# Optimization experiments

Hardware: AMD Instinct MI355X
Metric: run time of the kernel (lower is better)

The kernel has to match this reference:

```python
import jax, jax.numpy as jnp
import numpy as np

N_NODES = 16000
N_EDGES = 256000
F = 128        # invariant edge feature dim
MUL = 64       # multiplicity of env/V irreps (mul_gcd)
HID = 128      # mlp_n_hidden
SQRT3 = float(np.sqrt(3.0))

# e3nn-style activation normalization constant for silu:
# c = sqrt(E_{z~N(0,1)}[silu(z)^2]), so silu(z)/c has unit second moment.
_z = np.linspace(-12.0, 12.0, 100001)
_pdf = np.exp(-0.5 * _z ** 2) / np.sqrt(2.0 * np.pi)
_silu = _z / (1.0 + np.exp(-_z))
SILU_C = float(np.sqrt(np.trapz(_silu ** 2 * _pdf, _z)))


def _nsilu(x):
    return jax.nn.silu(x) / SILU_C


def _lin(x, W):
    # e3nn 'path' gradient normalization: W ~ N(0,1), forward scaled by 1/sqrt(fan_in)
    return (x @ W) / jnp.sqrt(jnp.asarray(W.shape[0], x.dtype))


def setup_inputs() -> dict:
    key = jax.random.key(0)
    ks = jax.random.split(key, 11)
    inp = {
        'vectors': jax.random.normal(ks[0], (N_EDGES, 3), jnp.float32),
        'x': jax.random.normal(ks[1], (N_EDGES, F), jnp.float32),
        'V': jax.random.normal(ks[2], (N_EDGES, 4 * MUL), jnp.float32),  # 64x0e + 64x1o
        'u': jax.random.uniform(ks[3], (N_EDGES,), jnp.float32),
        'm': jnp.ones((N_EDGES,), jnp.float32),
        'W_env': jax.random.normal(ks[4], (F, 2 * MUL), jnp.float32),
        'W1': jax.random.normal(ks[5], (F + 2 * MUL, HID), jnp.float32),
        'W2': jax.random.normal(ks[6], (HID, HID), jnp.float32),
        'W3': jax.random.normal(ks[7], (HID, HID), jnp.float32),
        'W_out': jax.random.normal(ks[8], (2 * MUL, MUL), jnp.float32),
        'senders': jax.random.randint(ks[9], (N_EDGES,), 0, N_NODES, jnp.int32),
    }
    return inp


def reference(vectors, x, V, u, m, W_env, W1, W2, W3, W_out, senders):
    E = vectors.shape[0]
    x = x * m[:, None]

    # n_neighbors = scatter_sum(m, dst=senders, map_back=True)
    n_neighbors = jax.ops.segment_sum(m, senders, num_segments=N_NODES)[senders]  # (E,)

    # w = Linear(num_irreps=2*MUL)(x)
    w = _lin(x, W_env)                  # (E, 128)
    w0, w1 = w[:, :MUL], w[:, MUL:]     # scalar / vector channel weights

    # spherical harmonics (component normalization): Y0 = 1, Y1 = sqrt(3)*rhat
    rhat = vectors / jnp.linalg.norm(vectors, axis=-1, keepdims=True)
    Y1 = SQRT3 * rhat                   # (E, 3)

    # w * Y * m, scatter_sum over senders, map back, normalize by n_neighbors
    denom = n_neighbors + 1e-5
    ws = w0 * m[:, None]                                   # (E, MUL)   w * Y0
    wv = (w1[:, :, None] * Y1[:, None, :]) * m[:, None, None]  # (E, MUL, 3)
    wY_s = jax.ops.segment_sum(ws, senders, num_segments=N_NODES)[senders] / denom[:, None]
    wY_v = jax.ops.segment_sum(wv, senders, num_segments=N_NODES)[senders] / denom[:, None, None]

    # V.mul_to_axis(): (E, MUL, 0e+1o)
    Vs = V[:, :MUL]                      # (E, MUL)
    Vv = V[:, MUL:].reshape(E, MUL, 3)   # (E, MUL, 3)

    # tensor product, filter_ir_out = {0e, 1o} (CG, component normalization)
    s_a = wY_s * Vs                                  # 0e x 0e -> 0e
    s_b = jnp.sum(wY_v * Vv, axis=-1) / SQRT3        # 1o x 1o -> 0e
    v_a = wY_s[:, :, None] * Vv                      # 0e x 1o -> 1o
    v_b = wY_v * Vs[:, :, None]                      # 1o x 0e -> 1o

    # scalars -> concatenated into x; vectors stay equivariant
    x = jnp.concatenate([x, s_a, s_b], axis=1)       # (E, F + 2*MUL)

    # invariant MLP (silu, no output activation)
    h = _nsilu(_lin(x, W1))
    h = _nsilu(_lin(h, W2))
    h = _lin(h, W3)                                  # (E, HID)
    x_out = u[:, None] * h

    # Linear(irreps_out=64x1o) on 128x1o
    V_in = jnp.concatenate([v_a, v_b], axis=1)       # (E, 2*MUL, 3)
    V_out = jnp.einsum('euk,uo->eok', V_in, W_out) / jnp.sqrt(jnp.asarray(2 * MUL, V.dtype))
    V_out = V_out.reshape(E, MUL * 3)                # (E, 192)

    return x_out, V_out
```

## Files before the change

### kernel.cpp

```cpp
#include <hip/hip_runtime.h>
#include <math.h>

typedef short bf16x8 __attribute__((ext_vector_type(8)));
typedef float f32x4 __attribute__((ext_vector_type(4)));

#define S128 0.08838834764831845f
#define S256I 0.0625f
#define NN_NODES 16000

#define WS_COUNTS   16448000
#define WS_OFFSETS  (WS_COUNTS + 64000)
#define WS_CURSOR   (WS_OFFSETS + 64000)
#define WS_INV      (WS_CURSOR + 64000)
#define WS_W1 (WS_INV + 1024000)
#define WS_W2 (WS_W1 + 65536)
#define WS_W3 (WS_W2 + 32768)
#define WS_WO (WS_W3 + 32768)
#define WS_WE (WS_WO + 16384)
#define WS_VECM (WS_WE + 32768)
#define WS_XMB  (WS_VECM + 4096000)

static float compute_inv_silu_c() {
    double sum = 0.0, prev = 0.0;
    const double dz = 24.0 / 100000.0;
    for (int i = 0; i <= 100000; ++i) {
        double z = -12.0 + dz * (double)i;
        double pdf = exp(-0.5 * z * z) * 0.3989422804014327;
        double s = z / (1.0 + exp(-z));
        double f = s * s * pdf;
        if (i) sum += 0.5 * (prev + f) * dz;
        prev = f;
    }
    return (float)(1.0 / sqrt(sum));
}
static const float INV_SILU_C = compute_inv_silu_c();

__device__ __forceinline__ unsigned int packbf(float a, float b) {
    union { float f; unsigned int u; } ca, cb;
    ca.f = a; cb.f = b;
    unsigned int ua = ca.u + (0x7fffu + ((ca.u >> 16) & 1u));
    unsigned int ub = cb.u + (0x7fffu + ((cb.u >> 16) & 1u));
    return (ua >> 16) | (ub & 0xffff0000u);
}
__device__ __forceinline__ unsigned short bf16r(float v) {
    union { float f; unsigned int u; } c; c.f = v;
    return (unsigned short)((c.u + (0x7fffu + ((c.u >> 16) & 1u))) >> 16);
}
__device__ __forceinline__ float bflo(unsigned int u) { return __uint_as_float(u << 16); }
__device__ __forceinline__ float bfhi(unsigned int u) { return __uint_as_float(u & 0xffff0000u); }
__device__ __forceinline__ int swz(int row, int b) { return b ^ ((row & 15) << 4); }
__device__ __forceinline__ float nsilu(float v, float ic) {
    return v / (1.0f + __expf(-v)) * ic;
}

__global__ __launch_bounds__(256) void k_wprep(
    const float* __restrict__ W1, const float* __restrict__ W2,
    const float* __restrict__ W3, const float* __restrict__ Wout,
    const float* __restrict__ Wenv, char* __restrict__ wsb)
{
    const int t = blockIdx.x * 256 + threadIdx.x;
    if (t < NN_NODES) ((int*)(wsb + WS_COUNTS))[t] = 0;
    if (t < 32768) {
        int n = t & 127, k = t >> 7;
        *(unsigned short*)(wsb + WS_W1 + n * 512 + k * 2) =
            bf16r(W1[k * 128 + n] * S256I);
    }
    if (t < 16384) {
        int n = t & 127, k = t >> 7;
        *(unsigned short*)(wsb + WS_W2 + n * 256 + k * 2) =
            bf16r(W2[k * 128 + n] * S128);
        *(unsigned short*)(wsb + WS_W3 + n * 256 + k * 2) =
            bf16r(W3[k * 128 + n] * S128);
    }
    if (t < 16384) {
        int j = t & 127, k = t >> 7;
        int c = (j & 1) ? 64 + (j >> 1) : (j >> 1);
        *(unsigned short*)(wsb + WS_WE + j * 256 + k * 2) =
            bf16r(Wenv[k * 128 + c] * S128);
    }
    if (t < 8192) {
        int o = t & 63, uu = t >> 6;
        *(unsigned short*)(wsb + WS_WO + o * 256 + ((uu * 2) ^ ((o & 15) << 4))) =
            bf16r(Wout[uu * 64 + o] * S128);
    }
}

__global__ __launch_bounds__(1024) void k_hist(
    const int* __restrict__ senders, int* __restrict__ counts, int E)
{
    const int e = blockIdx.x * 1024 + threadIdx.x;
    if (e < E) atomicAdd(&counts[senders[e]], 1);
}

__global__ __launch_bounds__(1024) void k_scan(
    const int* __restrict__ counts, int* __restrict__ offsets,
    int* __restrict__ cursor)
{
    __shared__ int part[1024];
    const int t = threadIdx.x;
    const int s0 = t * 16;
    const int s1 = (s0 + 16 < NN_NODES) ? s0 + 16 : NN_NODES;
    int s = 0;
    for (int i = s0; i < s1; ++i) s += counts[i];
    part[t] = s;
    __syncthreads();
    for (int off = 1; off < 1024; off <<= 1) {
        int v = part[t];
        if (t >= off) v += part[t - off];
        __syncthreads();
        part[t] = v;
        __syncthreads();
    }
    int run = t ? part[t - 1] : 0;
    for (int i = s0; i < s1; ++i) {
        offsets[i] = run; cursor[i] = run; run += counts[i];
    }
}

__global__ __launch_bounds__(1024) void k_binfill(
    const int* __restrict__ senders, const float* __restrict__ vectors,
    const float* __restrict__ m, int* __restrict__ cursor,
    int* __restrict__ inv, float4* __restrict__ vecm, int E)
{
    const int e = blockIdx.x * 1024 + threadIdx.x;
    if (e < E) {
        const int p = atomicAdd(&cursor[senders[e]], 1);
        inv[e] = p;
        float4 vm;
        vm.x = vectors[(size_t)e * 3 + 0];
        vm.y = vectors[(size_t)e * 3 + 1];
        vm.z = vectors[(size_t)e * 3 + 2];
        vm.w = m[e];
        vecm[p] = vm;
    }
}

__global__ __launch_bounds__(512) void k_env(
    const float* __restrict__ x, const float* __restrict__ m,
    const char* __restrict__ wsb, const int* __restrict__ inv,
    char* __restrict__ wout, char* __restrict__ xmb, int E)
{
    __shared__ char lds[32768];
    const int tid = threadIdx.x, l = tid & 63, wid = tid >> 6;
    const int lr = l & 15, lg = l >> 4;
    const int n0 = wid * 16;

    bf16x8 B[4];
    #pragma unroll
    for (int kk = 0; kk < 4; ++kk)
        B[kk] = *(const bf16x8*)(wsb + WS_WE + (n0 + lr) * 256 + kk * 64 + lg * 16);

    const int eb = blockIdx.x * 128;
    {
        const int el = tid >> 2, q = tid & 3;
        const int e = eb + el;
        if (e < E) {
            const float mv = m[e];
            const float4* xp = (const float4*)&x[(size_t)e * 128 + q * 32];
            #pragma unroll
            for (int j = 0; j < 4; ++j) {
                float4 A = xp[2 * j], Bv = xp[2 * j + 1];
                int4 w;
                w.x = packbf(A.x * mv, A.y * mv); w.y = packbf(A.z * mv, A.w * mv);
                w.z = packbf(Bv.x * mv, Bv.y * mv); w.w = packbf(Bv.z * mv, Bv.w * mv);
                *(int4*)(lds + el * 256 + swz(el, q * 64 + j * 16)) = w;
            }
        } else {
            const int4 z = {0, 0, 0, 0};
            #pragma unroll
            for (int j = 0; j < 4; ++j)
                *(int4*)(lds + el * 256 + swz(el, q * 64 + j * 16)) = z;
        }
    }
    __syncthreads();

    {
        const int el = tid >> 2, q = tid & 3;
        const int e = eb + el;
        if (e < E) {
            int4* d = (int4*)(xmb + (size_t)e * 256 + q * 64);
            #pragma unroll
            for (int j = 0; j < 4; ++j)
                d[j] = *(int4*)(lds + el * 256 + swz(el, q * 64 + j * 16));
        }
    }

    f32x4 acc[8];
    #pragma unroll
    for (int a = 0; a < 8; ++a) acc[a] = (f32x4){0.f, 0.f, 0.f, 0.f};

    #pragma unroll
    for (int kk = 0; kk < 4; ++kk) {
        const int kb = kk * 64 + lg * 16;
        #pragma unroll
        for (int mt = 0; mt < 8; ++mt) {
            const int row = mt * 16 + lr;
            bf16x8 a = *(const bf16x8*)(lds + row * 256 + swz(row, kb));
            acc[mt] = __builtin_amdgcn_mfma_f32_16x16x32_bf16(a, B[kk], acc[mt], 0, 0, 0);
        }
    }
    __syncthreads();

    #pragma unroll
    for (int mt = 0; mt < 8; ++mt)
        #pragma unroll
        for (int r = 0; r < 4; ++r) {
            const int row = mt * 16 + lg * 4 + r;
            *(unsigned short*)(lds + row * 256 + swz(row, (n0 + lr) * 2)) =
                bf16r(acc[mt][r]);
        }
    __syncthreads();

    {
        const int el = tid >> 2, q = tid & 3;
        const int e = eb + el;
        if (e < E) {
            const int p = inv[e];
            int4* d = (int4*)(wout + (size_t)p * 256 + q * 64);
            #pragma unroll
            for (int j = 0; j < 4; ++j)
                d[j] = *(int4*)(lds + el * 256 + swz(el, q * 64 + j * 16));
        }
    }
}

__global__ __launch_bounds__(256) void k_gather(
    const char* __restrict__ wvb, const float4* __restrict__ vecm,
    const int* __restrict__ counts, const int* __restrict__ offsets,
    float* __restrict__ node_cnt, float* __restrict__ node_s,
    float* __restrict__ node_v)
{
    const int l = threadIdx.x & 63, wid = threadIdx.x >> 6;
    const int n = blockIdx.x * 4 + wid;
    if (n >= NN_NODES) return;
    const int cnt = counts[n], base = offsets[n];

    float as = 0.f, a0 = 0.f, a1 = 0.f, a2 = 0.f, am = 0.f;
    for (int i = 0; i < cnt; ++i) {
        const unsigned int wv =
            *(const unsigned int*)(wvb + (size_t)(base + i) * 256 + l * 4);
        const float4 vm = vecm[base + i];
        const float rn = 1.7320508075688772f /
                         sqrtf(vm.x * vm.x + vm.y * vm.y + vm.z * vm.z);
        const float w0 = bflo(wv) * vm.w;
        const float c1 = bfhi(wv) * vm.w * rn;
        as += w0; am += vm.w;
        a0 += c1 * vm.x; a1 += c1 * vm.y; a2 += c1 * vm.z;
    }
    if (l == 0) node_cnt[n] = am;
    node_s[(size_t)n * 64 + l] = as;
    float* nv = &node_v[((size_t)n * 64 + l) * 3];
    nv[0] = a0; nv[1] = a1; nv[2] = a2;
}

__global__ __launch_bounds__(512, 4) void k_fuse(
    const float* __restrict__ V, const int* __restrict__ senders,
    const float* __restrict__ node_cnt, const float* __restrict__ node_s,
    const float* __restrict__ node_v, const char* __restrict__ wsb,
    const char* __restrict__ xmb, const float* __restrict__ ug,
    float* __restrict__ out_x, float* __restrict__ out_v,
    float inv_c, int E)
{
    __shared__ char lds[81920];
    const int tid = threadIdx.x, l = tid & 63, wid = tid >> 6;
    const int lr = l & 15, lg = l >> 4;
    const int eb = blockIdx.x * 64;

    {
        const int4* src = (const int4*)(wsb + WS_WO);
        ((int4*)(lds + 49152))[tid * 2]     = src[tid * 2];
        ((int4*)(lds + 49152))[tid * 2 + 1] = src[tid * 2 + 1];
    }

    #pragma unroll 2
    for (int i = 0; i < 8; ++i) {
        const int el = wid * 8 + i;
        const int e  = eb + el;
        float Vs = 0.f, Vv0 = 0.f, Vv1 = 0.f, Vv2 = 0.f;
        float wYs = 0.f, wv0 = 0.f, wv1 = 0.f, wv2 = 0.f;
        if (e < E) {
            Vs = V[(size_t)e * 256 + l];
            const float* vp = &V[(size_t)e * 256 + 64 + l * 3];
            Vv0 = vp[0]; Vv1 = vp[1]; Vv2 = vp[2];
            const int sn = senders[e];
            const float rden = 1.0f / (node_cnt[sn] + 1e-5f);
            wYs = node_s[(size_t)sn * 64 + l] * rden;
            const float* nvp = &node_v[((size_t)sn * 64 + l) * 3];
            wv0 = nvp[0] * rden; wv1 = nvp[1] * rden; wv2 = nvp[2] * rden;
        }
        *(unsigned short*)(lds + 65536 + el * 256 + swz(el, l * 2)) =
            bf16r(wYs * Vs);
        *(unsigned short*)(lds + 65536 + el * 256 + swz(el, 128 + l * 2)) =
            bf16r((wv0 * Vv0 + wv1 * Vv1 + wv2 * Vv2) * 0.57735026918962576f);
        const float vvk[3] = {Vv0, Vv1, Vv2};
        const float wvk[3] = {wv0, wv1, wv2};
        #pragma unroll
        for (int k = 0; k < 3; ++k) {
            const int row = el * 3 + k;
            *(unsigned short*)(lds + row * 256 + swz(row, l * 2))       = bf16r(wYs * vvk[k]);
            *(unsigned short*)(lds + row * 256 + swz(row, 128 + l * 2)) = bf16r(wvk[k] * Vs);
        }
    }
    __syncthreads();

    {
        const int wm = wid & 3, wn = wid >> 2;
        const int m0 = wm * 48, n0v = wn * 32;
        f32x4 acc[3][2];
        #pragma unroll
        for (int a = 0; a < 3; ++a)
            #pragma unroll
            for (int b = 0; b < 2; ++b) acc[a][b] = (f32x4){0.f, 0.f, 0.f, 0.f};

        #pragma unroll
        for (int kk = 0; kk < 4; ++kk) {
            const int kb = kk * 64 + lg * 16;
            bf16x8 a0 = *(const bf16x8*)(lds + (m0 + lr) * 256      + swz(m0 + lr, kb));
            bf16x8 a1 = *(const bf16x8*)(lds + (m0 + 16 + lr) * 256 + swz(m0 + 16 + lr, kb));
            bf16x8 a2 = *(const bf16x8*)(lds + (m0 + 32 + lr) * 256 + swz(m0 + 32 + lr, kb));
            bf16x8 b0 = *(const bf16x8*)(lds + 49152 + (n0v + lr) * 256      + swz(n0v + lr, kb));
            bf16x8 b1 = *(const bf16x8*)(lds + 49152 + (n0v + 16 + lr) * 256 + swz(n0v + 16 + lr, kb));
            acc[0][0] = __builtin_amdgcn_mfma_f32_16x16x32_bf16(a0, b0, acc[0][0], 0, 0, 0);
            acc[0][1] = __builtin_amdgcn_mfma_f32_16x16x32_bf16(a0, b1, acc[0][1], 0, 0, 0);
            acc[1][0] = __builtin_amdgcn_mfma_f32_16x16x32_bf16(a1, b0, acc[1][0], 0, 0, 0);
            acc[1][1] = __builtin_amdgcn_mfma_f32_16x16x32_bf16(a1, b1, acc[1][1], 0, 0, 0);
            acc[2][0] = __builtin_amdgcn_mfma_f32_16x16x32_bf16(a2, b0, acc[2][0], 0, 0, 0);
            acc[2][1] = __builtin_amdgcn_mfma_f32_16x16x32_bf16(a2, b1, acc[2][1], 0, 0, 0);
        }
        __syncthreads();

        #pragma unroll
        for (int mt = 0; mt < 3; ++mt)
            #pragma unroll
            for (int nt = 0; nt < 2; ++nt)
                #pragma unroll
                for (int r = 0; r < 4; ++r) {
                    const int mm = m0 + mt * 16 + lg * 4 + r;
                    const int el2 = mm / 3, kd = mm - el2 * 3;
                    const int o = n0v + nt * 16 + lr;
                    *(float*)(lds + el2 * 768 + (o * 3 + kd) * 4) = acc[mt][nt][r];
                }
    }
    __syncthreads();
    if (eb + 64 <= E) {
        const int4* s = (const int4*)lds;
        int4* d = (int4*)(out_v + (size_t)eb * 192);
        #pragma unroll
        for (int j = 0; j < 6; ++j) d[tid * 6 + j] = s[tid * 6 + j];
    } else {
        for (int idx = tid; idx < 64 * 192; idx += 512) {
            const int el2 = idx / 192;
            if (eb + el2 < E)
                out_v[(size_t)(eb + el2) * 192 + (idx % 192)] = *(float*)(lds + idx * 4);
        }
    }
    __syncthreads();

    const int n0 = wid * 16;
    bf16x8 B1[8];
    #pragma unroll
    for (int kk = 0; kk < 8; ++kk)
        B1[kk] = *(const bf16x8*)(wsb + WS_W1 + (n0 + lr) * 512 + kk * 64 + lg * 16);

    {
        const int el = tid >> 3, q = tid & 7;
        const int e = eb + el;
        int4 x0, x1;
        if (e < E) {
            const int4* xp = (const int4*)(xmb + (size_t)e * 256 + q * 32);
            x0 = xp[0]; x1 = xp[1];
        } else {
            x0 = (int4){0, 0, 0, 0}; x1 = (int4){0, 0, 0, 0};
        }
        *(int4*)(lds + el * 256 + swz(el, q * 32))      = x0;
        *(int4*)(lds + el * 256 + swz(el, q * 32 + 16)) = x1;
    }
    __syncthreads();

    f32x4 a1[4];
    #pragma unroll
    for (int a = 0; a < 4; ++a) a1[a] = (f32x4){0.f, 0.f, 0.f, 0.f};
    #pragma unroll
    for (int kk = 0; kk < 8; ++kk) {
        const int base = (kk < 4) ? 0 : 65536;
        const int kb = (kk & 3) * 64 + lg * 16;
        #pragma unroll
        for (int mt = 0; mt < 4; ++mt) {
            const int row = mt * 16 + lr;
            bf16x8 a = *(const bf16x8*)(lds + base + row * 256 + swz(row, kb));
            a1[mt] = __builtin_amdgcn_mfma_f32_16x16x32_bf16(a, B1[kk], a1[mt], 0, 0, 0);
        }
    }

    bf16x8 B2[4], B3[4];
    #pragma unroll
    for (int kk = 0; kk < 4; ++kk) {
        B2[kk] = *(const bf16x8*)(wsb + WS_W2 + (n0 + lr) * 256 + kk * 64 + lg * 16);
        B3[kk] = *(const bf16x8*)(wsb + WS_W3 + (n0 + lr) * 256 + kk * 64 + lg * 16);
    }

    #pragma unroll
    for (int mt = 0; mt < 4; ++mt)
        #pragma unroll
        for (int r = 0; r < 4; ++r) {
            const int row = mt * 16 + lg * 4 + r;
            *(unsigned short*)(lds + 32768 + row * 256 + swz(row, (n0 + lr) * 2)) =
                bf16r(nsilu(a1[mt][r], inv_c));
        }
    __syncthreads();

    f32x4 a2[4];
    #pragma unroll
    for (int a = 0; a < 4; ++a) a2[a] = (f32x4){0.f, 0.f, 0.f, 0.f};
    #pragma unroll
    for (int kk = 0; kk < 4; ++kk) {
        const int kb = kk * 64 + lg * 16;
        #pragma unroll
        for (int mt = 0; mt < 4; ++mt) {
            const int row = mt * 16 + lr;
            bf16x8 a = *(const bf16x8*)(lds + 32768 + row * 256 + swz(row, kb));
            a2[mt] = __builtin_amdgcn_mfma_f32_16x16x32_bf16(a, B2[kk], a2[mt], 0, 0, 0);
        }
    }
    #pragma unroll
    for (int mt = 0; mt < 4; ++mt)
        #pragma unroll
        for (int r = 0; r < 4; ++r) {
            const int row = mt * 16 + lg * 4 + r;
            *(unsigned short*)(lds + row * 256 + swz(row, (n0 + lr) * 2)) =
                bf16r(nsilu(a2[mt][r], inv_c));
        }
    __syncthreads();

    f32x4 a3[4];
    #pragma unroll
    for (int a = 0; a < 4; ++a) a3[a] = (f32x4){0.f, 0.f, 0.f, 0.f};
    #pragma unroll
    for (int kk = 0; kk < 4; ++kk) {
        const int kb = kk * 64 + lg * 16;
        #pragma unroll
        for (int mt = 0; mt < 4; ++mt) {
            const int row = mt * 16 + lr;
            bf16x8 a = *(const bf16x8*)(lds + row * 256 + swz(row, kb));
            a3[mt] = __builtin_amdgcn_mfma_f32_16x16x32_bf16(a, B3[kk], a3[mt], 0, 0, 0);
        }
    }
    __syncthreads();

    {
        const int base = (n0 < 64) ? 0 : 16384;
        const int colb = n0 & 63;
        #pragma unroll
        for (int mt = 0; mt < 4; ++mt)
            #pragma unroll
            for (int r = 0; r < 4; ++r) {
                const int row = mt * 16 + lg * 4 + r;
                *(float*)(lds + base + row * 256 + swz(row, (colb + lr) * 4)) = a3[mt][r];
            }
    }
    __syncthreads();

    {
        const int el = tid >> 3, q = tid & 7;
        const int e = eb + el;
        if (e < E) {
            const float uu = ug[e];
            #pragma unroll
            for (int j = 0; j < 4; ++j) {
                const int b = q * 64 + j * 16;
                const int base = (b < 256) ? 0 : 16384;
                int4 v = *(int4*)(lds + base + el * 256 + swz(el, b & 255));
                float4 f;
                f.x = __int_as_float(v.x) * uu; f.y = __int_as_float(v.y) * uu;
                f.z = __int_as_float(v.z) * uu; f.w = __int_as_float(v.w) * uu;
                *(float4*)(&out_x[(size_t)e * 128 + q * 16 + j * 4]) = f;
            }
        }
    }
}

extern "C" void kernel_launch(void* const* d_in, const int* in_sizes, int n_in,
                              void* d_out, int out_size, void* d_ws, size_t ws_size,
                              hipStream_t stream) {
    const float* vectors = (const float*)d_in[0];
    const float* x       = (const float*)d_in[1];
    const float* V       = (const float*)d_in[2];
    const float* u       = (const float*)d_in[3];
    const float* m       = (const float*)d_in[4];
    const float* W_env   = (const float*)d_in[5];
    const float* W1      = (const float*)d_in[6];
    const float* W2      = (const float*)d_in[7];
    const float* W3      = (const float*)d_in[8];
    const float* W_out   = (const float*)d_in[9];
    const int*   senders = (const int*)d_in[10];

    const int E = in_sizes[4];

    char*  wsb      = (char*)d_ws;
    float* node_cnt = (float*)d_ws;
    float* node_s   = node_cnt + NN_NODES;
    float* node_v   = node_s + (size_t)NN_NODES * 64;
    int* counts  = (int*)(wsb + WS_COUNTS);
    int* offsets = (int*)(wsb + WS_OFFSETS);
    int* cursor  = (int*)(wsb + WS_CURSOR);
    int* inv     = (int*)(wsb + WS_INV);
    float4* vecm = (float4*)(wsb + WS_VECM);
    char* xmb    = wsb + WS_XMB;

    float* out_x = (float*)d_out;
    float* out_v = out_x + (size_t)E * 128;
    char*  wvb   = (char*)out_v;

    k_wprep<<<128, 256, 0, stream>>>(W1, W2, W3, W_out, W_env, wsb);
    k_hist<<<(E + 1023) / 1024, 1024, 0, stream>>>(senders, counts, E);
    k_scan<<<1, 1024, 0, stream>>>(counts, offsets, cursor);
    k_binfill<<<(E + 1023) / 1024, 1024, 0, stream>>>(senders, vectors, m,
                                                      cursor, inv, vecm, E);
    k_env<<<(E + 127) / 128, 512, 0, stream>>>(x, m, wsb, inv, wvb, xmb, E);
    k_gather<<<(NN_NODES + 3) / 4, 256, 0, stream>>>(wvb, vecm, counts, offsets,
                                                     node_cnt, node_s, node_v);
    k_fuse<<<(E + 63) / 64, 512, 0, stream>>>(V, senders, node_cnt, node_s,
                                              node_v, wsb, xmb, u,
                                              out_x, out_v, INV_SILU_C, E);
}
```

Before: 429.4 us.

## Batch gather loads, store MLP output directly, unroll node gather loop

In the fused kernel, all eight edges' V and node-aggregate loads are issued up front into register arrays before any LDS writes, so more memory requests are in flight at once. The final LDS staging and the two barriers before the output write are removed; each lane now writes its MFMA accumulator values straight to global memory, scaled by u. The node gather loop gets an unroll pragma. Direct stores are scalar and less coalesced (16 lanes write contiguous floats per row), and the extra live registers may raise pressure under the 512-thread, 4-block launch bound.

```diff
diff --git a/kernel.cpp b/kernel.cpp
--- a/kernel.cpp
+++ b/kernel.cpp
@@ -236,6 +236,7 @@
     const int cnt = counts[n], base = offsets[n];
 
     float as = 0.f, a0 = 0.f, a1 = 0.f, a2 = 0.f, am = 0.f;
+    #pragma unroll 4
     for (int i = 0; i < cnt; ++i) {
         const unsigned int wv =
             *(const unsigned int*)(wvb + (size_t)(base + i) * 256 + l * 4);
@@ -272,34 +273,37 @@
         ((int4*)(lds + 49152))[tid * 2 + 1] = src[tid * 2 + 1];
     }
 
-    #pragma unroll 2
+    float vs[8], v0[8], v1[8], v2[8], ws[8], w0[8], w1[8], w2[8];
+    #pragma unroll
+    for (int i = 0; i < 8; ++i) {
+        const int e = eb + wid * 8 + i;
+        vs[i] = 0.f; v0[i] = 0.f; v1[i] = 0.f; v2[i] = 0.f;
+        ws[i] = 0.f; w0[i] = 0.f; w1[i] = 0.f; w2[i] = 0.f;
+        if (e < E) {
+            vs[i] = V[(size_t)e * 256 + l];
+            const float* vp = &V[(size_t)e * 256 + 64 + l * 3];
+            v0[i] = vp[0]; v1[i] = vp[1]; v2[i] = vp[2];
+            const int sn = senders[e];
+            const float rden = 1.0f / (node_cnt[sn] + 1e-5f);
+            ws[i] = node_s[(size_t)sn * 64 + l] * rden;
+            const float* nvp = &node_v[((size_t)sn * 64 + l) * 3];
+            w0[i] = nvp[0] * rden; w1[i] = nvp[1] * rden; w2[i] = nvp[2] * rden;
+        }
+    }
+    #pragma unroll
     for (int i = 0; i < 8; ++i) {
         const int el = wid * 8 + i;
-        const int e  = eb + el;
-        float Vs = 0.f, Vv0 = 0.f, Vv1 = 0.f, Vv2 = 0.f;
-        float wYs = 0.f, wv0 = 0.f, wv1 = 0.f, wv2 = 0.f;
-        if (e < E) {
-            Vs = V[(size_t)e * 256 + l];
-            const float* vp = &V[(size_t)e * 256 + 64 + l * 3];
-            Vv0 = vp[0]; Vv1 = vp[1]; Vv2 = vp[2];
-            const int sn = senders[e];
-            const float rden = 1.0f / (node_cnt[sn] + 1e-5f);
-            wYs = node_s[(size_t)sn * 64 + l] * rden;
-            const float* nvp = &node_v[((size_t)sn * 64 + l) * 3];
-            wv0 = nvp[0] * rden; wv1 = nvp[1] * rden; wv2 = nvp[2] * rden;
-        }
         *(unsigned short*)(lds + 65536 + el * 256 + swz(el, l * 2)) =
-            bf16r(wYs * Vs);
+            bf16r(ws[i] * vs[i]);
         *(unsigned short*)(lds + 65536 + el * 256 + swz(el, 128 + l * 2)) =
-            bf16r((wv0 * Vv0 + wv1 * Vv1 + wv2 * Vv2) * 0.57735026918962576f);
-        const float vvk[3] = {Vv0, Vv1, Vv2};
-        const float wvk[3] = {wv0, wv1, wv2};
-        #pragma unroll
-        for (int k = 0; k < 3; ++k) {
-            const int row = el * 3 + k;
-            *(unsigned short*)(lds + row * 256 + swz(row, l * 2))       = bf16r(wYs * vvk[k]);
-            *(unsigned short*)(lds + row * 256 + swz(row, 128 + l * 2)) = bf16r(wvk[k] * Vs);
-        }
+            bf16r((w0[i] * v0[i] + w1[i] * v1[i] + w2[i] * v2[i]) * 0.57735026918962576f);
+        const int r0 = el * 3;
+        *(unsigned short*)(lds + r0 * 256 + swz(r0, l * 2))             = bf16r(ws[i] * v0[i]);
+        *(unsigned short*)(lds + r0 * 256 + swz(r0, 128 + l * 2))       = bf16r(w0[i] * vs[i]);
+        *(unsigned short*)(lds + (r0 + 1) * 256 + swz(r0 + 1, l * 2))       = bf16r(ws[i] * v1[i]);
+        *(unsigned short*)(lds + (r0 + 1) * 256 + swz(r0 + 1, 128 + l * 2)) = bf16r(w1[i] * vs[i]);
+        *(unsigned short*)(lds + (r0 + 2) * 256 + swz(r0 + 2, l * 2))       = bf16r(ws[i] * v2[i]);
+        *(unsigned short*)(lds + (r0 + 2) * 256 + swz(r0 + 2, 128 + l * 2)) = bf16r(w2[i] * vs[i]);
     }
     __syncthreads();
 
@@ -445,38 +449,15 @@
             a3[mt] = __builtin_amdgcn_mfma_f32_16x16x32_bf16(a, B3[kk], a3[mt], 0, 0, 0);
         }
     }
-    __syncthreads();
-
-    {
-        const int base = (n0 < 64) ? 0 : 16384;
-        const int colb = n0 & 63;
-        #pragma unroll
-        for (int mt = 0; mt < 4; ++mt)
-            #pragma unroll
-            for (int r = 0; r < 4; ++r) {
-                const int row = mt * 16 + lg * 4 + r;
-                *(float*)(lds + base + row * 256 + swz(row, (colb + lr) * 4)) = a3[mt][r];
-            }
-    }
-    __syncthreads();
-
-    {
-        const int el = tid >> 3, q = tid & 7;
-        const int e = eb + el;
-        if (e < E) {
-            const float uu = ug[e];
-            #pragma unroll
-            for (int j = 0; j < 4; ++j) {
-                const int b = q * 64 + j * 16;
-                const int base = (b < 256) ? 0 : 16384;
-                int4 v = *(int4*)(lds + base + el * 256 + swz(el, b & 255));
-                float4 f;
-                f.x = __int_as_float(v.x) * uu; f.y = __int_as_float(v.y) * uu;
-                f.z = __int_as_float(v.z) * uu; f.w = __int_as_float(v.w) * uu;
-                *(float4*)(&out_x[(size_t)e * 128 + q * 16 + j * 4]) = f;
-            }
-        }
-    }
+    #pragma unroll
+    for (int mt = 0; mt < 4; ++mt)
+        #pragma unroll
+        for (int r = 0; r < 4; ++r) {
+            const int row = mt * 16 + lg * 4 + r;
+            const int e = eb + row;
+            if (e < E)
+                out_x[(size_t)e * 128 + n0 + lr] = ug[e] * a3[mt][r];
+        }
 }
 
 extern "C" void kernel_launch(void* const* d_in, const int* in_sizes, int n_in,
```

Result: slower. 438.2 us (+2.1%).

## Process edges in sender-sorted order in fused kernel for node-data locality

Applied to the files above, without the earlier changes.

k_fuse now iterates over edges in sender-sorted order, using a new order array filled in k_binfill. The masked x buffer is written in sorted position by k_env. Consecutive edges in a block then share senders, so node_s and node_v reads become cache-friendly instead of random. In exchange, the reads of V and u and the stores to out_x and out_v become scattered per edge row. The gather loop also gets an unroll pragma.

```diff
diff --git a/kernel.cpp b/kernel.cpp
--- a/kernel.cpp
+++ b/kernel.cpp
@@ -19,6 +19,7 @@
 #define WS_WE (WS_WO + 16384)
 #define WS_VECM (WS_WE + 32768)
 #define WS_XMB  (WS_VECM + 4096000)
+#define WS_ORDER (WS_XMB + 65536000)
 
 static float compute_inv_silu_c() {
     double sum = 0.0, prev = 0.0;
@@ -120,12 +121,14 @@
 __global__ __launch_bounds__(1024) void k_binfill(
     const int* __restrict__ senders, const float* __restrict__ vectors,
     const float* __restrict__ m, int* __restrict__ cursor,
-    int* __restrict__ inv, float4* __restrict__ vecm, int E)
+    int* __restrict__ inv, int* __restrict__ order,
+    float4* __restrict__ vecm, int E)
 {
     const int e = blockIdx.x * 1024 + threadIdx.x;
     if (e < E) {
         const int p = atomicAdd(&cursor[senders[e]], 1);
         inv[e] = p;
+        order[p] = e;
         float4 vm;
         vm.x = vectors[(size_t)e * 3 + 0];
         vm.y = vectors[(size_t)e * 3 + 1];
@@ -178,7 +181,8 @@
         const int el = tid >> 2, q = tid & 3;
         const int e = eb + el;
         if (e < E) {
-            int4* d = (int4*)(xmb + (size_t)e * 256 + q * 64);
+            const int p = inv[e];
+            int4* d = (int4*)(xmb + (size_t)p * 256 + q * 64);
             #pragma unroll
             for (int j = 0; j < 4; ++j)
                 d[j] = *(int4*)(lds + el * 256 + swz(el, q * 64 + j * 16));
@@ -236,6 +240,7 @@
     const int cnt = counts[n], base = offsets[n];
 
     float as = 0.f, a0 = 0.f, a1 = 0.f, a2 = 0.f, am = 0.f;
+    #pragma unroll 4
     for (int i = 0; i < cnt; ++i) {
         const unsigned int wv =
             *(const unsigned int*)(wvb + (size_t)(base + i) * 256 + l * 4);
@@ -258,13 +263,14 @@
     const float* __restrict__ node_cnt, const float* __restrict__ node_s,
     const float* __restrict__ node_v, const char* __restrict__ wsb,
     const char* __restrict__ xmb, const float* __restrict__ ug,
+    const int* __restrict__ order,
     float* __restrict__ out_x, float* __restrict__ out_v,
     float inv_c, int E)
 {
     __shared__ char lds[81920];
     const int tid = threadIdx.x, l = tid & 63, wid = tid >> 6;
     const int lr = l & 15, lg = l >> 4;
-    const int eb = blockIdx.x * 64;
+    const int pbase = blockIdx.x * 64;
 
     {
         const int4* src = (const int4*)(wsb + WS_WO);
@@ -275,10 +281,11 @@
     #pragma unroll 2
     for (int i = 0; i < 8; ++i) {
         const int el = wid * 8 + i;
-        const int e  = eb + el;
+        const int p  = pbase + el;
         float Vs = 0.f, Vv0 = 0.f, Vv1 = 0.f, Vv2 = 0.f;
         float wYs = 0.f, wv0 = 0.f, wv1 = 0.f, wv2 = 0.f;
-        if (e < E) {
+        if (p < E) {
+            const int e = order[p];
             Vs = V[(size_t)e * 256 + l];
             const float* vp = &V[(size_t)e * 256 + 64 + l * 3];
             Vv0 = vp[0]; Vv1 = vp[1]; Vv2 = vp[2];
@@ -342,16 +349,15 @@
                 }
     }
     __syncthreads();
-    if (eb + 64 <= E) {
-        const int4* s = (const int4*)lds;
-        int4* d = (int4*)(out_v + (size_t)eb * 192);
-        #pragma unroll
-        for (int j = 0; j < 6; ++j) d[tid * 6 + j] = s[tid * 6 + j];
-    } else {
-        for (int idx = tid; idx < 64 * 192; idx += 512) {
-            const int el2 = idx / 192;
-            if (eb + el2 < E)
-                out_v[(size_t)(eb + el2) * 192 + (idx % 192)] = *(float*)(lds + idx * 4);
+    {
+        const int el = tid >> 3, q = tid & 7;
+        const int p = pbase + el;
+        if (p < E) {
+            const int e = order[p];
+            const int4* s = (const int4*)(lds + el * 768 + q * 96);
+            int4* d = (int4*)(out_v + (size_t)e * 192 + q * 24);
+            #pragma unroll
+            for (int j = 0; j < 6; ++j) d[j] = s[j];
         }
     }
     __syncthreads();
@@ -364,10 +370,10 @@
 
     {
         const int el = tid >> 3, q = tid & 7;
-        const int e = eb + el;
+        const int p = pbase + el;
         int4 x0, x1;
-        if (e < E) {
-            const int4* xp = (const int4*)(xmb + (size_t)e * 256 + q * 32);
+        if (p < E) {
+            const int4* xp = (const int4*)(xmb + (size_t)p * 256 + q * 32);
             x0 = xp[0]; x1 = xp[1];
         } else {
             x0 = (int4){0, 0, 0, 0}; x1 = (int4){0, 0, 0, 0};
@@ -462,8 +468,9 @@
 
     {
         const int el = tid >> 3, q = tid & 7;
-        const int e = eb + el;
-        if (e < E) {
+        const int p = pbase + el;
+        if (p < E) {
+            const int e = order[p];
             const float uu = ug[e];
             #pragma unroll
             for (int j = 0; j < 4; ++j) {
@@ -504,6 +511,7 @@
     int* offsets = (int*)(wsb + WS_OFFSETS);
     int* cursor  = (int*)(wsb + WS_CURSOR);
     int* inv     = (int*)(wsb + WS_INV);
+    int* order   = (int*)(wsb + WS_ORDER);
     float4* vecm = (float4*)(wsb + WS_VECM);
     char* xmb    = wsb + WS_XMB;
 
@@ -515,11 +523,11 @@
     k_hist<<<(E + 1023) / 1024, 1024, 0, stream>>>(senders, counts, E);
     k_scan<<<1, 1024, 0, stream>>>(counts, offsets, cursor);
     k_binfill<<<(E + 1023) / 1024, 1024, 0, stream>>>(senders, vectors, m,
-                                                      cursor, inv, vecm, E);
+                                                      cursor, inv, order, vecm, E);
     k_env<<<(E + 127) / 128, 512, 0, stream>>>(x, m, wsb, inv, wvb, xmb, E);
     k_gather<<<(NN_NODES + 3) / 4, 256, 0, stream>>>(wvb, vecm, counts, offsets,
                                                      node_cnt, node_s, node_v);
     k_fuse<<<(E + 63) / 64, 512, 0, stream>>>(V, senders, node_cnt, node_s,
-                                              node_v, wsb, xmb, u,
+                                              node_v, wsb, xmb, u, order,
                                               out_x, out_v, INV_SILU_C, E);
 }
```

New measurement: 451.9 us. +5.2%, slower.
